# Kernel optimization log

Hardware: AMD Instinct MI355X
Metric: run time of the kernel (lower is better)

Reference implementation:

```python
import jax, jax.numpy as jnp
import numpy as np

B, S, D, OUT = 4, 4096, 256, 64
SCALE = 1.0 / np.sqrt(64.0)  # module hard-codes / 64**0.5


def setup_inputs() -> dict:
    key = jax.random.key(0)
    k1, k2 = jax.random.split(key)
    x = jax.random.normal(k1, (B, S, D), dtype=jnp.float32)
    kernel = jax.random.normal(k2, (3, D, OUT), dtype=jnp.float32) * 0.05
    return {"x": x, "kernel": kernel}


def reference(x, kernel):
    # Single-head attention with shared-input Q/K/V projections.
    q = jnp.einsum('bsd,do->bso', x, kernel[0])
    k = jnp.einsum('bsd,do->bso', x, kernel[1])
    v = jnp.einsum('bsd,do->bso', x, kernel[2])
    scores = jnp.einsum('bqo,bko->bqk', q, k) * SCALE  # [B,S,S]
    attn = jax.nn.softmax(scores, axis=-1)
    return jnp.einsum('bqk,bko->bqo', attn, v)  # [B,S,OUT]
```

## Files before the change

### kernel.cpp

```cpp
#include <hip/hip_runtime.h>

#define SLEN 4096
#define NB 4
#define DIN 256
#define DOUT 64
#define KVSPLIT 4
#define KVBLK 64
#define QBLK 128
#define NT ((SLEN / KVSPLIT) / KVBLK)

typedef _Float16 f16;
typedef _Float16 f16x8 __attribute__((ext_vector_type(8)));
typedef _Float16 f16x4 __attribute__((ext_vector_type(4)));
typedef float f32x4 __attribute__((ext_vector_type(4)));

#define QSCALE 0.1803368801111204f
#define PSHIFT2 4.328085122666891f

#define GLD16(gsrc, ldst)                                          \
  __builtin_amdgcn_global_load_lds(                                \
      (const __attribute__((address_space(1))) void*)(gsrc),       \
      (__attribute__((address_space(3))) void*)(ldst), 16, 0, 0)

__global__ __launch_bounds__(256) void setup_kernel(
    const float* __restrict__ w, f16* __restrict__ wth,
    float* __restrict__ out, float* __restrict__ pL) {
  int gtid = blockIdx.x * 256 + threadIdx.x;
  if (gtid < 3 * DIN * DOUT) {
    int m = gtid / (DIN * DOUT);
    int r = gtid - m * (DIN * DOUT);
    int k = r >> 6, o = r & 63;
    wth[(m * DOUT + o) * DIN + k] = (f16)w[gtid];
  }
  const int ntot = NB * SLEN * DOUT;
  for (int i = gtid; i < ntot + NB * SLEN; i += 65536) {
    if (i < ntot) out[i] = 0.f;
    else pL[i - ntot] = 0.f;
  }
}

__global__ __launch_bounds__(64) void proj_kernel(
    const float* __restrict__ x, const f16* __restrict__ wth,
    f16* __restrict__ qh, f16* __restrict__ kh, f16* __restrict__ vth) {
  __shared__ alignas(16) f16 tbuf[64 * 24];
  const int lane = threadIdx.x;
  const int c = lane & 15, g = lane >> 4;
  const int m = blockIdx.y;
  const int tb = blockIdx.x * 16;
  const int b = tb >> 12, s0 = tb & 4095;

  f16x8 a[8];
  {
    const float* xr = x + (size_t)(tb + c) * DIN + g * 8;
#pragma unroll
    for (int ks = 0; ks < 8; ++ks) {
      f32x4 lo = *(const f32x4*)(xr + ks * 32);
      f32x4 hi = *(const f32x4*)(xr + ks * 32 + 4);
      f16x8 av;
#pragma unroll
      for (int j = 0; j < 4; ++j) { av[j] = (f16)lo[j]; av[j + 4] = (f16)hi[j]; }
      a[ks] = av;
    }
  }

  const f16* wb = wth + (size_t)m * DOUT * DIN + (size_t)c * DIN + g * 8;
  f32x4 acc[4];
#pragma unroll
  for (int nt = 0; nt < 4; ++nt) acc[nt] = (f32x4){0.f, 0.f, 0.f, 0.f};
#pragma unroll
  for (int ks = 0; ks < 8; ++ks)
#pragma unroll
    for (int nt = 0; nt < 4; ++nt) {
      f16x8 bf = *(const f16x8*)(wb + (size_t)(nt * 16) * DIN + ks * 32);
      acc[nt] = __builtin_amdgcn_mfma_f32_16x16x32_f16(a[ks], bf, acc[nt], 0, 0, 0);
    }

  if (m < 2) {
#pragma unroll
    for (int nt = 0; nt < 4; ++nt)
#pragma unroll
      for (int rr = 0; rr < 4; ++rr)
        tbuf[(4 * g + rr) * 72 + nt * 16 + c] =
            (f16)(m == 0 ? acc[nt][rr] * QSCALE : acc[nt][rr]);
    const int rw = lane >> 2, cb = (lane & 3) * 16;
    f16x8 r0 = *(const f16x8*)&tbuf[rw * 72 + cb];
    f16x8 r1 = *(const f16x8*)&tbuf[rw * 72 + cb + 8];
    f16* dst = (m == 0 ? qh : kh) + (size_t)(tb + rw) * DOUT + cb;
    *(f16x8*)(dst) = r0;
    *(f16x8*)(dst + 8) = r1;
  } else {
#pragma unroll
    for (int nt = 0; nt < 4; ++nt)
#pragma unroll
      for (int rr = 0; rr < 4; ++rr)
        tbuf[(nt * 16 + c) * 24 + 4 * g + rr] = (f16)acc[nt][rr];
    f16x8 r0 = *(const f16x8*)&tbuf[lane * 24];
    f16x8 r1 = *(const f16x8*)&tbuf[lane * 24 + 8];
    f16* dst = vth + ((size_t)b * DOUT + lane) * SLEN + s0;
    *(f16x8*)(dst) = r0;
    *(f16x8*)(dst + 8) = r1;
  }
}

__global__ __launch_bounds__(256, 3) void attn_kernel(
    const f16* __restrict__ qh, const f16* __restrict__ kh,
    const f16* __restrict__ vth, float* __restrict__ out,
    float* __restrict__ pL) {
  __shared__ alignas(16) f16 kb[2][KVBLK * 64];
  __shared__ alignas(16) f16 vb[2][KVBLK * 64];
  __shared__ alignas(16) f16 pbuf[4][32 * 64];

  const int tid = threadIdx.x;
  const int lane = tid & 63;
  const int c = lane & 15, g = lane >> 4;
  const int wv = tid >> 6;

  const int wg = ((blockIdx.x & 7) << 6) + (blockIdx.x >> 3);
  const int b = wg >> 7;
  const int split = (wg >> 5) & 3;
  const int qb = wg & 31;
  const int q0 = qb * QBLK + wv * 32;
  const int kv0 = split * (SLEN / KVSPLIT);

  f16* plds = pbuf[wv];

  const int srow = tid >> 3;
  const int scol = (tid & 7) * 8;
  const f16* kgbase = kh + (size_t)b * SLEN * DOUT;
  const f16* vgbase = vth + (size_t)b * DOUT * SLEN;

  f16x8 qf[4];
#pragma unroll
  for (int h = 0; h < 2; ++h) {
    const f16* qr = qh + ((size_t)(b * SLEN + q0 + 16 * h + c)) * DOUT + g * 8;
    qf[2 * h] = *(const f16x8*)(qr);
    qf[2 * h + 1] = *(const f16x8*)(qr + 32);
  }

  f32x4 o0[4], o1[4];
#pragma unroll
  for (int nt = 0; nt < 4; ++nt) {
    o0[nt] = (f32x4){0.f, 0.f, 0.f, 0.f};
    o1[nt] = (f32x4){0.f, 0.f, 0.f, 0.f};
  }
  float lr0 = 0.f, lr1 = 0.f;

  auto stage = [&](int sel, int kv) {
#pragma unroll
    for (int rr = 0; rr < 2; ++rr) {
      int r = srow + rr * 32;
      int sw = scol ^ ((r & 7) << 3);
      GLD16(kgbase + (size_t)(kv + r) * DOUT + sw,
            (char*)(&kb[sel][0]) + wv * 1024 + rr * 4096);
      GLD16(vgbase + (size_t)r * SLEN + kv + sw,
            (char*)(&vb[sel][0]) + wv * 1024 + rr * 4096);
    }
  };

  stage(0, kv0);
  __syncthreads();

  for (int t = 0; t < NT; ++t) {
    const int sel = t & 1;
    if (t + 1 < NT) stage(sel ^ 1, kv0 + (t + 1) * KVBLK);

    f32x4 s0[4], s1[4];
    __builtin_amdgcn_s_setprio(1);
#pragma unroll
    for (int t4 = 0; t4 < 4; ++t4) {
      f16x8 k0 = *(const f16x8*)&kb[sel][(16 * t4 + c) * 64 + 8 * (g ^ (c & 7))];
      f16x8 k1 = *(const f16x8*)&kb[sel][(16 * t4 + c) * 64 + 8 * ((g + 4) ^ (c & 7))];
      f32x4 z = (f32x4){0.f, 0.f, 0.f, 0.f};
      s0[t4] = __builtin_amdgcn_mfma_f32_16x16x32_f16(k0, qf[0], z, 0, 0, 0);
      s0[t4] = __builtin_amdgcn_mfma_f32_16x16x32_f16(k1, qf[1], s0[t4], 0, 0, 0);
      s1[t4] = __builtin_amdgcn_mfma_f32_16x16x32_f16(k0, qf[2], z, 0, 0, 0);
      s1[t4] = __builtin_amdgcn_mfma_f32_16x16x32_f16(k1, qf[3], s1[t4], 0, 0, 0);
    }
    __builtin_amdgcn_s_setprio(0);

    f16x4 pk0[4], pk1[4];
#pragma unroll
    for (int t4 = 0; t4 < 4; ++t4)
#pragma unroll
      for (int r = 0; r < 4; ++r) {
        float p0 = exp2f(s0[t4][r] - PSHIFT2);
        float p1 = exp2f(s1[t4][r] - PSHIFT2);
        lr0 += p0;
        lr1 += p1;
        pk0[t4][r] = (f16)p0;
        pk1[t4][r] = (f16)p1;
      }

#pragma unroll
    for (int t4 = 0; t4 < 4; ++t4) {
      int sw = (16 * t4 + 4 * g) ^ ((c & 7) << 3);
      *(f16x4*)&plds[c * 64 + sw] = pk0[t4];
      *(f16x4*)&plds[1024 + c * 64 + sw] = pk1[t4];
    }

    __builtin_amdgcn_s_setprio(1);
#pragma unroll
    for (int s2 = 0; s2 < 2; ++s2) {
      int sw = (s2 * 32 + g * 8) ^ ((c & 7) << 3);
      f16x8 pa0 = *(const f16x8*)&plds[c * 64 + sw];
      f16x8 pa1 = *(const f16x8*)&plds[1024 + c * 64 + sw];
#pragma unroll
      for (int nt = 0; nt < 4; ++nt) {
        f16x8 vf = *(const f16x8*)&vb[sel][(16 * nt + c) * 64 + 8 * ((g + 4 * s2) ^ (c & 7))];
        o0[nt] = __builtin_amdgcn_mfma_f32_16x16x32_f16(pa0, vf, o0[nt], 0, 0, 0);
        o1[nt] = __builtin_amdgcn_mfma_f32_16x16x32_f16(pa1, vf, o1[nt], 0, 0, 0);
      }
    }
    __builtin_amdgcn_s_setprio(0);

    __syncthreads();
  }

  const size_t rowb = (size_t)b * SLEN + q0;
#pragma unroll
  for (int nt = 0; nt < 4; ++nt)
#pragma unroll
    for (int r = 0; r < 4; ++r) {
      atomicAdd(&out[(rowb + 4 * g + r) * DOUT + nt * 16 + c], o0[nt][r]);
      atomicAdd(&out[(rowb + 16 + 4 * g + r) * DOUT + nt * 16 + c], o1[nt][r]);
    }
  lr0 += __shfl_xor(lr0, 16);
  lr0 += __shfl_xor(lr0, 32);
  lr1 += __shfl_xor(lr1, 16);
  lr1 += __shfl_xor(lr1, 32);
  if (lane < 16) {
    atomicAdd(&pL[rowb + lane], lr0);
    atomicAdd(&pL[rowb + 16 + lane], lr1);
  }
}

__global__ __launch_bounds__(256) void norm_kernel(
    float* __restrict__ out, const float* __restrict__ pL) {
  int i = blockIdx.x * 256 + threadIdx.x;
  int row = i >> 4;
  float rl = 1.0f / pL[row];
  f32x4 o = *(const f32x4*)&out[(size_t)i * 4];
  o *= rl;
  *(f32x4*)&out[(size_t)i * 4] = o;
}

extern "C" void kernel_launch(void* const* d_in, const int* in_sizes, int n_in,
                              void* d_out, int out_size, void* d_ws, size_t ws_size,
                              hipStream_t stream) {
  const float* x = (const float*)d_in[0];
  const float* w = (const float*)d_in[1];
  float* out = (float*)d_out;

  const size_t NE = (size_t)NB * SLEN * DOUT;
  f16* qh = (f16*)d_ws;
  f16* kh = qh + NE;
  f16* vth = kh + NE;
  f16* wth = vth + NE;
  float* pL = (float*)(wth + 3 * DIN * DOUT);

  hipLaunchKernelGGL(setup_kernel, dim3(256), dim3(256), 0, stream,
                     w, wth, out, pL);
  hipLaunchKernelGGL(proj_kernel, dim3(NB * SLEN / 16, 3), dim3(64), 0, stream,
                     x, wth, qh, kh, vth);
  hipLaunchKernelGGL(attn_kernel, dim3(NB * KVSPLIT * (SLEN / QBLK)), dim3(256),
                     0, stream, qh, kh, vth, out, pL);
  hipLaunchKernelGGL(norm_kernel, dim3(NB * SLEN * DOUT / 4 / 256), dim3(256),
                     0, stream, out, pL);
}
```

Before: 127.6 us.

## Use 512-thread attention blocks with wider Q tile, more KV splits, folded shift

```diff
diff --git a/kernel.cpp b/kernel.cpp
--- a/kernel.cpp
+++ b/kernel.cpp
@@ -4,18 +4,24 @@
 #define NB 4
 #define DIN 256
 #define DOUT 64
-#define KVSPLIT 4
+#define KVSPLIT 8
 #define KVBLK 64
-#define QBLK 128
-#define NT ((SLEN / KVSPLIT) / KVBLK)
+#define QBLK 256
+#define CHUNK (SLEN / KVSPLIT)
+#define NT (CHUNK / KVBLK)
 
 typedef _Float16 f16;
 typedef _Float16 f16x8 __attribute__((ext_vector_type(8)));
 typedef _Float16 f16x4 __attribute__((ext_vector_type(4)));
+typedef _Float16 f16x2 __attribute__((ext_vector_type(2)));
 typedef float f32x4 __attribute__((ext_vector_type(4)));
 
 #define QSCALE 0.1803368801111204f
 #define PSHIFT2 4.328085122666891f
+
+static __device__ __forceinline__ f16x2 pkrtz(float a, float b) {
+  return __builtin_bit_cast(f16x2, __builtin_amdgcn_cvt_pkrtz(a, b));
+}
 
 #define GLD16(gsrc, ldst)                                          \
   __builtin_amdgcn_global_load_lds(                                \
@@ -102,13 +108,13 @@
   }
 }
 
-__global__ __launch_bounds__(256, 3) void attn_kernel(
+__global__ __launch_bounds__(512, 4) void attn_kernel(
     const f16* __restrict__ qh, const f16* __restrict__ kh,
     const f16* __restrict__ vth, float* __restrict__ out,
     float* __restrict__ pL) {
   __shared__ alignas(16) f16 kb[2][KVBLK * 64];
   __shared__ alignas(16) f16 vb[2][KVBLK * 64];
-  __shared__ alignas(16) f16 pbuf[4][32 * 64];
+  __shared__ alignas(16) f16 pbuf[8][32 * 64];
 
   const int tid = threadIdx.x;
   const int lane = tid & 63;
@@ -117,10 +123,11 @@
 
   const int wg = ((blockIdx.x & 7) << 6) + (blockIdx.x >> 3);
   const int b = wg >> 7;
-  const int split = (wg >> 5) & 3;
-  const int qb = wg & 31;
+  const int w128 = wg & 127;
+  const int split = w128 >> 4;
+  const int qb = w128 & 15;
   const int q0 = qb * QBLK + wv * 32;
-  const int kv0 = split * (SLEN / KVSPLIT);
+  const int kv0 = split * CHUNK;
 
   f16* plds = pbuf[wv];
 
@@ -144,22 +151,20 @@
     o1[nt] = (f32x4){0.f, 0.f, 0.f, 0.f};
   }
   float lr0 = 0.f, lr1 = 0.f;
+  const f32x4 zinit = (f32x4){-PSHIFT2, -PSHIFT2, -PSHIFT2, -PSHIFT2};
 
   auto stage = [&](int sel, int kv) {
-#pragma unroll
-    for (int rr = 0; rr < 2; ++rr) {
-      int r = srow + rr * 32;
-      int sw = scol ^ ((r & 7) << 3);
-      GLD16(kgbase + (size_t)(kv + r) * DOUT + sw,
-            (char*)(&kb[sel][0]) + wv * 1024 + rr * 4096);
-      GLD16(vgbase + (size_t)r * SLEN + kv + sw,
-            (char*)(&vb[sel][0]) + wv * 1024 + rr * 4096);
-    }
+    int sw = scol ^ ((srow & 7) << 3);
+    GLD16(kgbase + (size_t)(kv + srow) * DOUT + sw,
+          (char*)(&kb[sel][0]) + wv * 1024);
+    GLD16(vgbase + (size_t)srow * SLEN + kv + sw,
+          (char*)(&vb[sel][0]) + wv * 1024);
   };
 
   stage(0, kv0);
   __syncthreads();
 
+#pragma unroll 2
   for (int t = 0; t < NT; ++t) {
     const int sel = t & 1;
     if (t + 1 < NT) stage(sel ^ 1, kv0 + (t + 1) * KVBLK);
@@ -170,26 +175,27 @@
     for (int t4 = 0; t4 < 4; ++t4) {
       f16x8 k0 = *(const f16x8*)&kb[sel][(16 * t4 + c) * 64 + 8 * (g ^ (c & 7))];
       f16x8 k1 = *(const f16x8*)&kb[sel][(16 * t4 + c) * 64 + 8 * ((g + 4) ^ (c & 7))];
-      f32x4 z = (f32x4){0.f, 0.f, 0.f, 0.f};
-      s0[t4] = __builtin_amdgcn_mfma_f32_16x16x32_f16(k0, qf[0], z, 0, 0, 0);
+      s0[t4] = __builtin_amdgcn_mfma_f32_16x16x32_f16(k0, qf[0], zinit, 0, 0, 0);
       s0[t4] = __builtin_amdgcn_mfma_f32_16x16x32_f16(k1, qf[1], s0[t4], 0, 0, 0);
-      s1[t4] = __builtin_amdgcn_mfma_f32_16x16x32_f16(k0, qf[2], z, 0, 0, 0);
+      s1[t4] = __builtin_amdgcn_mfma_f32_16x16x32_f16(k0, qf[2], zinit, 0, 0, 0);
       s1[t4] = __builtin_amdgcn_mfma_f32_16x16x32_f16(k1, qf[3], s1[t4], 0, 0, 0);
     }
     __builtin_amdgcn_s_setprio(0);
 
     f16x4 pk0[4], pk1[4];
 #pragma unroll
-    for (int t4 = 0; t4 < 4; ++t4)
-#pragma unroll
-      for (int r = 0; r < 4; ++r) {
-        float p0 = exp2f(s0[t4][r] - PSHIFT2);
-        float p1 = exp2f(s1[t4][r] - PSHIFT2);
-        lr0 += p0;
-        lr1 += p1;
-        pk0[t4][r] = (f16)p0;
-        pk1[t4][r] = (f16)p1;
-      }
+    for (int t4 = 0; t4 < 4; ++t4) {
+      float e00 = exp2f(s0[t4][0]), e01 = exp2f(s0[t4][1]);
+      float e02 = exp2f(s0[t4][2]), e03 = exp2f(s0[t4][3]);
+      float e10 = exp2f(s1[t4][0]), e11 = exp2f(s1[t4][1]);
+      float e12 = exp2f(s1[t4][2]), e13 = exp2f(s1[t4][3]);
+      lr0 += (e00 + e01) + (e02 + e03);
+      lr1 += (e10 + e11) + (e12 + e13);
+      f16x2 a0 = pkrtz(e00, e01), a1 = pkrtz(e02, e03);
+      f16x2 b0 = pkrtz(e10, e11), b1 = pkrtz(e12, e13);
+      pk0[t4] = (f16x4){a0[0], a0[1], a1[0], a1[1]};
+      pk1[t4] = (f16x4){b0[0], b0[1], b1[0], b1[1]};
+    }
 
 #pragma unroll
     for (int t4 = 0; t4 < 4; ++t4) {
@@ -262,7 +268,7 @@
                      w, wth, out, pL);
   hipLaunchKernelGGL(proj_kernel, dim3(NB * SLEN / 16, 3), dim3(64), 0, stream,
                      x, wth, qh, kh, vth);
-  hipLaunchKernelGGL(attn_kernel, dim3(NB * KVSPLIT * (SLEN / QBLK)), dim3(256),
+  hipLaunchKernelGGL(attn_kernel, dim3(NB * KVSPLIT * (SLEN / QBLK)), dim3(512),
                      0, stream, qh, kh, vth, out, pL);
   hipLaunchKernelGGL(norm_kernel, dim3(NB * SLEN * DOUT / 4 / 256), dim3(256),
                      0, stream, out, pL);
```

Measured after the change: 140.3 us. 1.1x slower.
